# Optimization experiments

Hardware: AMD Instinct MI355X
Metric: run time of the kernel (lower is better)

Reference implementation:

```python
import jax, jax.numpy as jnp
import numpy as np

N_NODES = 50000
N_EDGES = 600000
D_IN = 128
D_OUT = 128


def setup_inputs() -> dict:
    key = jax.random.key(0)
    ks = jax.random.split(key, 6)
    gain = float(np.sqrt(2.0))  # relu gain for xavier init
    lim = gain * np.sqrt(6.0 / (D_IN + D_IN))
    pool_w = jax.random.uniform(ks[0], (D_IN, D_IN), jnp.float32, -lim, lim)
    lim2 = gain * np.sqrt(6.0 / (D_IN + D_OUT))
    lin_w = jax.random.uniform(ks[1], (D_OUT, D_IN), jnp.float32, -lim2, lim2)
    return {
        "node_feats": jax.random.normal(ks[2], (N_NODES, D_IN), jnp.float32),
        "src": jax.random.randint(ks[3], (N_EDGES,), 0, N_NODES, jnp.int32),
        "dst": jax.random.randint(ks[4], (N_EDGES,), 0, N_NODES, jnp.int32),
        "e_weight": jax.random.uniform(ks[5], (N_EDGES,), jnp.float32),
        "pool_w": pool_w,
        "pool_b": jnp.zeros((D_IN,), jnp.float32),
        "lin_w": lin_w,
        "lin_b": jnp.zeros((D_OUT,), jnp.float32),
        "bias": jnp.zeros((D_OUT,), jnp.float32),
    }


def reference(node_feats, src, dst, e_weight, pool_w, pool_b, lin_w, lin_b, bias):
    # maxpool aggregator: h_src = relu(pool(x) + pool_bias)   [N, D_IN]
    h_src = jax.nn.relu(node_feats @ pool_w.T + pool_b)
    # u_mul_e message: gather src features, scale by edge weight  [E, D_IN]
    m = h_src[src] * e_weight[:, None]
    # fn.max reduce per destination node; empty mailboxes -> 0
    h_new = jax.ops.segment_max(m, dst, num_segments=N_NODES)
    h_new = jnp.where(jnp.isfinite(h_new), h_new, 0.0)
    # final linear (+its bias) + extra bias parameter
    return h_new @ lin_w.T + lin_b + bias
```

## Files before the change

### kernel.cpp

```cpp
#include <hip/hip_runtime.h>
#include <hip/hip_bf16.h>

#define NN 50000
#define NE 600000
#define DD 128
#define CAP 48

typedef __attribute__((ext_vector_type(8))) short short8_t;
typedef __attribute__((ext_vector_type(4))) short short4_t;
typedef __attribute__((ext_vector_type(4))) float f32x4;

__device__ __forceinline__ short f2bf(float f) {
    union { float f; unsigned u; } v; v.f = f;
    unsigned r = (v.u + 0x7FFFu + ((v.u >> 16) & 1u)) >> 16;
    return (short)r;
}
__device__ __forceinline__ float bflo(unsigned x) { return __uint_as_float(x << 16); }
__device__ __forceinline__ float bfhi(unsigned x) { return __uint_as_float(x & 0xffff0000u); }

template<bool RELU, bool B2, bool IN_BF, bool OUT_BF>
__global__ __launch_bounds__(512) void gemm128(const void* __restrict__ Av,
        const float* __restrict__ W, const float* __restrict__ b1,
        const float* __restrict__ b2, void* __restrict__ outv, int M,
        int* __restrict__ zbuf)
{
    __shared__ short aL[128 * 128];
    __shared__ short wL[128 * 128];
    const int tid = threadIdx.x;
    const int m0 = blockIdx.x * 128;

    if (zbuf) {
        int gid = blockIdx.x * 512 + tid;
        if (gid < NN) zbuf[gid] = 0;
    }

    if (IN_BF) {
        const unsigned short* A = (const unsigned short*)Av;
        #pragma unroll
        for (int i = 0; i < 4; ++i) {
            int flat = i * 4096 + tid * 8;
            int row = flat >> 7, k = flat & 127;
            int gr = m0 + row;
            short8_t s8 = {0,0,0,0,0,0,0,0};
            if (gr < M) s8 = *(const short8_t*)(A + (size_t)gr * 128 + k);
            *(short8_t*)(aL + ((row * 128 + k) ^ ((row & 7) << 3))) = s8;
        }
    } else {
        const float* A = (const float*)Av;
        #pragma unroll
        for (int i = 0; i < 8; ++i) {
            int flat = i * 2048 + tid * 4;
            int row = flat >> 7, k = flat & 127;
            int gr = m0 + row;
            float4 v = make_float4(0.f, 0.f, 0.f, 0.f);
            if (gr < M) v = *(const float4*)(A + (size_t)gr * 128 + k);
            short4_t s4 = { f2bf(v.x), f2bf(v.y), f2bf(v.z), f2bf(v.w) };
            *(short4_t*)(aL + ((row * 128 + k) ^ ((row & 7) << 3))) = s4;
        }
    }
    #pragma unroll
    for (int i = 0; i < 8; ++i) {
        int flat = i * 2048 + tid * 4;
        int row = flat >> 7, k = flat & 127;
        float4 v = *(const float4*)(W + flat);
        short4_t s4 = { f2bf(v.x), f2bf(v.y), f2bf(v.z), f2bf(v.w) };
        *(short4_t*)(wL + ((row * 128 + k) ^ ((row & 7) << 3))) = s4;
    }
    __syncthreads();

    const int lane = tid & 63, wid = tid >> 6;
    const int l15 = lane & 15, lhi = lane >> 4;
    const int r0 = wid * 16;
    f32x4 acc[8];
    #pragma unroll
    for (int t = 0; t < 8; ++t) acc[t] = f32x4{0.f, 0.f, 0.f, 0.f};

    #pragma unroll
    for (int kk = 0; kk < 4; ++kk) {
        const int k0 = kk * 32 + lhi * 8;
        const int ar = r0 + l15;
        short8_t a = *(short8_t*)(aL + ((ar * 128 + k0) ^ ((ar & 7) << 3)));
        #pragma unroll
        for (int t = 0; t < 8; ++t) {
            const int br = t * 16 + l15;
            short8_t b = *(short8_t*)(wL + ((br * 128 + k0) ^ ((br & 7) << 3)));
            acc[t] = __builtin_amdgcn_mfma_f32_16x16x32_bf16(a, b, acc[t], 0, 0, 0);
        }
    }

    #pragma unroll
    for (int t = 0; t < 8; ++t) {
        const int c = t * 16 + l15;
        float add = b1[c];
        if (B2) add += b2[c];
        #pragma unroll
        for (int i = 0; i < 4; ++i) {
            int r = m0 + r0 + lhi * 4 + i;
            if (r < M) {
                float v = acc[t][i] + add;
                if (RELU) v = fmaxf(v, 0.f);
                if (OUT_BF) ((unsigned short*)outv)[(size_t)r * 128 + c] = (unsigned short)f2bf(v);
                else        ((float*)outv)[(size_t)r * 128 + c] = v;
            }
        }
    }
}

__global__ __launch_bounds__(256) void bucket(const int* __restrict__ src,
        const int* __restrict__ dst, const float* __restrict__ ew,
        int* __restrict__ counts, unsigned* __restrict__ edges)
{
    int e = blockIdx.x * 256 + threadIdx.x;
    if (e >= NE) return;
    int d = dst[e];
    int pos = atomicAdd(&counts[d], 1);
    if (pos < CAP)
        edges[(size_t)d * CAP + pos] =
            ((unsigned)src[e] << 16) | (unsigned short)f2bf(ew[e]);
}

__global__ __launch_bounds__(256) void node_max(const unsigned short* __restrict__ hb,
        const int* __restrict__ counts, const unsigned* __restrict__ edges,
        unsigned short* __restrict__ hnew)
{
    int node = blockIdx.x * 4 + (threadIdx.x >> 6);
    if (node >= NN) return;
    const int lane = threadIdx.x & 63;
    const int g = lane >> 4, l16 = lane & 15;
    const int deg = min(counts[node], CAP);
    const unsigned* ep = edges + (size_t)node * CAP;
    unsigned p = (lane < deg) ? ep[lane] : 0u;

    float m0=0.f,m1=0.f,m2=0.f,m3=0.f,m4=0.f,m5=0.f,m6=0.f,m7=0.f;
    for (int j = 0; j < deg; j += 8) {
        int ia = j + g, ib = j + 4 + g;
        unsigned pa = __shfl(p, ia & 63);
        unsigned pb = __shfl(p, ib & 63);
        float wa = (ia < deg) ? __uint_as_float(pa << 16) : 0.f;
        float wb = (ib < deg) ? __uint_as_float(pb << 16) : 0.f;
        uint4 ra = *(const uint4*)(hb + (size_t)(pa >> 16) * 128 + l16 * 8);
        uint4 rb = *(const uint4*)(hb + (size_t)(pb >> 16) * 128 + l16 * 8);
        m0 = fmaxf(m0, bflo(ra.x) * wa); m1 = fmaxf(m1, bfhi(ra.x) * wa);
        m2 = fmaxf(m2, bflo(ra.y) * wa); m3 = fmaxf(m3, bfhi(ra.y) * wa);
        m4 = fmaxf(m4, bflo(ra.z) * wa); m5 = fmaxf(m5, bfhi(ra.z) * wa);
        m6 = fmaxf(m6, bflo(ra.w) * wa); m7 = fmaxf(m7, bfhi(ra.w) * wa);
        m0 = fmaxf(m0, bflo(rb.x) * wb); m1 = fmaxf(m1, bfhi(rb.x) * wb);
        m2 = fmaxf(m2, bflo(rb.y) * wb); m3 = fmaxf(m3, bfhi(rb.y) * wb);
        m4 = fmaxf(m4, bflo(rb.z) * wb); m5 = fmaxf(m5, bfhi(rb.z) * wb);
        m6 = fmaxf(m6, bflo(rb.w) * wb); m7 = fmaxf(m7, bfhi(rb.w) * wb);
    }

    #define CMB(mm) mm = fmaxf(mm, __shfl_xor(mm, 16)); \
                    mm = fmaxf(mm, __shfl_xor(mm, 32));
    CMB(m0) CMB(m1) CMB(m2) CMB(m3) CMB(m4) CMB(m5) CMB(m6) CMB(m7)
    #undef CMB

    if (g == 0) {
        uint4 o;
        o.x = ((unsigned)(unsigned short)f2bf(m1) << 16) | (unsigned short)f2bf(m0);
        o.y = ((unsigned)(unsigned short)f2bf(m3) << 16) | (unsigned short)f2bf(m2);
        o.z = ((unsigned)(unsigned short)f2bf(m5) << 16) | (unsigned short)f2bf(m4);
        o.w = ((unsigned)(unsigned short)f2bf(m7) << 16) | (unsigned short)f2bf(m6);
        *(uint4*)(hnew + (size_t)node * 128 + l16 * 8) = o;
    }
}

extern "C" void kernel_launch(void* const* d_in, const int* in_sizes, int n_in,
                              void* d_out, int out_size, void* d_ws, size_t ws_size,
                              hipStream_t stream) {
    const float* node_feats = (const float*)d_in[0];
    const int*   src        = (const int*)d_in[1];
    const int*   dst        = (const int*)d_in[2];
    const float* ew         = (const float*)d_in[3];
    const float* pool_w     = (const float*)d_in[4];
    const float* pool_b     = (const float*)d_in[5];
    const float* lin_w      = (const float*)d_in[6];
    const float* lin_b      = (const float*)d_in[7];
    const float* bias       = (const float*)d_in[8];
    float* out = (float*)d_out;

    char* w0 = (char*)d_ws;
    unsigned short* hsrc = (unsigned short*)w0;  w0 += (size_t)NN * DD * 2;
    unsigned short* hnew = (unsigned short*)w0;  w0 += (size_t)NN * DD * 2;
    int* counts = (int*)w0;                      w0 += (size_t)NN * 4;
    unsigned* edges = (unsigned*)w0;             w0 += (size_t)NN * CAP * 4;

    const int gemm_grid = (NN + 127) / 128;
    gemm128<true, false, false, true><<<gemm_grid, 512, 0, stream>>>(node_feats,
            pool_w, pool_b, nullptr, hsrc, NN, counts);

    bucket<<<(NE + 255) / 256, 256, 0, stream>>>(src, dst, ew, counts, edges);

    node_max<<<(NN + 3) / 4, 256, 0, stream>>>(hsrc, counts, edges, hnew);

    gemm128<false, true, true, false><<<gemm_grid, 512, 0, stream>>>(hnew,
            lin_w, lin_b, bias, out, NN, nullptr);
}
```

Measured before the change: 167.8 us.

## Pre-convert weights to bf16, load GEMM operands into registers, unroll gather by degree

A new prep kernel converts both weight matrices to bf16 once and zeroes the per-node edge counters. The GEMM is rewritten to read A and B fragments straight from global memory into registers, dropping the LDS staging and barrier, and uses 64-row tiles with waves split across column halves. The node_max gather now runs a fully unrolled loop whose iteration count (2, 4 or 6) is picked by degree bucket, so more loads can be in flight. The costs are an extra kernel launch and redundant weight-fragment loads per wave that rely on the cache to absorb them.

Measured after the change: 195.9 us. 16.8% more time.

```diff
diff --git a/kernel.cpp b/kernel.cpp
--- a/kernel.cpp
+++ b/kernel.cpp
@@ -18,84 +18,86 @@
 __device__ __forceinline__ float bflo(unsigned x) { return __uint_as_float(x << 16); }
 __device__ __forceinline__ float bfhi(unsigned x) { return __uint_as_float(x & 0xffff0000u); }
 
+__global__ __launch_bounds__(256) void prep(const float* __restrict__ pw,
+        const float* __restrict__ lw, unsigned short* __restrict__ w1,
+        unsigned short* __restrict__ w2, int* __restrict__ counts)
+{
+    const int b = blockIdx.x, t = threadIdx.x;
+    if (b < 196) {
+        int i = b * 256 + t;
+        if (i < NN) counts[i] = 0;
+    } else if (b < 212) {
+        int base = (b - 196) * 1024 + t * 4;
+        float4 v = *(const float4*)(pw + base);
+        short4_t s4 = { f2bf(v.x), f2bf(v.y), f2bf(v.z), f2bf(v.w) };
+        *(short4_t*)(w1 + base) = s4;
+    } else {
+        int base = (b - 212) * 1024 + t * 4;
+        float4 v = *(const float4*)(lw + base);
+        short4_t s4 = { f2bf(v.x), f2bf(v.y), f2bf(v.z), f2bf(v.w) };
+        *(short4_t*)(w2 + base) = s4;
+    }
+}
+
 template<bool RELU, bool B2, bool IN_BF, bool OUT_BF>
-__global__ __launch_bounds__(512) void gemm128(const void* __restrict__ Av,
-        const float* __restrict__ W, const float* __restrict__ b1,
-        const float* __restrict__ b2, void* __restrict__ outv, int M,
-        int* __restrict__ zbuf)
-{
-    __shared__ short aL[128 * 128];
-    __shared__ short wL[128 * 128];
+__global__ __launch_bounds__(512) void gemmz(const void* __restrict__ Av,
+        const unsigned short* __restrict__ Wb, const float* __restrict__ b1,
+        const float* __restrict__ b2, void* __restrict__ outv, int M)
+{
     const int tid = threadIdx.x;
-    const int m0 = blockIdx.x * 128;
-
-    if (zbuf) {
-        int gid = blockIdx.x * 512 + tid;
-        if (gid < NN) zbuf[gid] = 0;
-    }
-
+    const int lane = tid & 63, wid = tid >> 6;
+    const int l15 = lane & 15, lhi = lane >> 4;
+    const int rg = wid & 3, cs = wid >> 2;
+    const int m0 = blockIdx.x * 64 + rg * 16;
+    const int ar = m0 + l15;
+
+    short8_t bf[4][4];
+    #pragma unroll
+    for (int t = 0; t < 4; ++t) {
+        const int br = cs * 64 + t * 16 + l15;
+        #pragma unroll
+        for (int kk = 0; kk < 4; ++kk)
+            bf[t][kk] = *(const short8_t*)(Wb + br * 128 + kk * 32 + lhi * 8);
+    }
+
+    short8_t af[4];
     if (IN_BF) {
         const unsigned short* A = (const unsigned short*)Av;
         #pragma unroll
-        for (int i = 0; i < 4; ++i) {
-            int flat = i * 4096 + tid * 8;
-            int row = flat >> 7, k = flat & 127;
-            int gr = m0 + row;
-            short8_t s8 = {0,0,0,0,0,0,0,0};
-            if (gr < M) s8 = *(const short8_t*)(A + (size_t)gr * 128 + k);
-            *(short8_t*)(aL + ((row * 128 + k) ^ ((row & 7) << 3))) = s8;
+        for (int kk = 0; kk < 4; ++kk)
+            af[kk] = *(const short8_t*)(A + (size_t)ar * 128 + kk * 32 + lhi * 8);
+    } else {
+        const int arc = min(ar, M - 1);
+        const float* A = (const float*)Av;
+        #pragma unroll
+        for (int kk = 0; kk < 4; ++kk) {
+            float4 u = *(const float4*)(A + (size_t)arc * 128 + kk * 32 + lhi * 8);
+            float4 v = *(const float4*)(A + (size_t)arc * 128 + kk * 32 + lhi * 8 + 4);
+            af[kk] = short8_t{ f2bf(u.x), f2bf(u.y), f2bf(u.z), f2bf(u.w),
+                               f2bf(v.x), f2bf(v.y), f2bf(v.z), f2bf(v.w) };
         }
-    } else {
-        const float* A = (const float*)Av;
-        #pragma unroll
-        for (int i = 0; i < 8; ++i) {
-            int flat = i * 2048 + tid * 4;
-            int row = flat >> 7, k = flat & 127;
-            int gr = m0 + row;
-            float4 v = make_float4(0.f, 0.f, 0.f, 0.f);
-            if (gr < M) v = *(const float4*)(A + (size_t)gr * 128 + k);
-            short4_t s4 = { f2bf(v.x), f2bf(v.y), f2bf(v.z), f2bf(v.w) };
-            *(short4_t*)(aL + ((row * 128 + k) ^ ((row & 7) << 3))) = s4;
-        }
-    }
-    #pragma unroll
-    for (int i = 0; i < 8; ++i) {
-        int flat = i * 2048 + tid * 4;
-        int row = flat >> 7, k = flat & 127;
-        float4 v = *(const float4*)(W + flat);
-        short4_t s4 = { f2bf(v.x), f2bf(v.y), f2bf(v.z), f2bf(v.w) };
-        *(short4_t*)(wL + ((row * 128 + k) ^ ((row & 7) << 3))) = s4;
-    }
-    __syncthreads();
-
-    const int lane = tid & 63, wid = tid >> 6;
-    const int l15 = lane & 15, lhi = lane >> 4;
-    const int r0 = wid * 16;
-    f32x4 acc[8];
-    #pragma unroll
-    for (int t = 0; t < 8; ++t) acc[t] = f32x4{0.f, 0.f, 0.f, 0.f};
+    }
+
+    f32x4 acc[4];
+    #pragma unroll
+    for (int t = 0; t < 4; ++t) acc[t] = f32x4{0.f, 0.f, 0.f, 0.f};
 
     #pragma unroll
     for (int kk = 0; kk < 4; ++kk) {
-        const int k0 = kk * 32 + lhi * 8;
-        const int ar = r0 + l15;
-        short8_t a = *(short8_t*)(aL + ((ar * 128 + k0) ^ ((ar & 7) << 3)));
-        #pragma unroll
-        for (int t = 0; t < 8; ++t) {
-            const int br = t * 16 + l15;
-            short8_t b = *(short8_t*)(wL + ((br * 128 + k0) ^ ((br & 7) << 3)));
-            acc[t] = __builtin_amdgcn_mfma_f32_16x16x32_bf16(a, b, acc[t], 0, 0, 0);
-        }
-    }
-
-    #pragma unroll
-    for (int t = 0; t < 8; ++t) {
-        const int c = t * 16 + l15;
+        #pragma unroll
+        for (int t = 0; t < 4; ++t)
+            acc[t] = __builtin_amdgcn_mfma_f32_16x16x32_bf16(af[kk], bf[t][kk],
+                                                             acc[t], 0, 0, 0);
+    }
+
+    #pragma unroll
+    for (int t = 0; t < 4; ++t) {
+        const int c = cs * 64 + t * 16 + l15;
         float add = b1[c];
         if (B2) add += b2[c];
         #pragma unroll
         for (int i = 0; i < 4; ++i) {
-            int r = m0 + r0 + lhi * 4 + i;
+            int r = m0 + lhi * 4 + i;
             if (r < M) {
                 float v = acc[t][i] + add;
                 if (RELU) v = fmaxf(v, 0.f);
@@ -119,6 +121,29 @@
             ((unsigned)src[e] << 16) | (unsigned short)f2bf(ew[e]);
 }
 
+template<int NIT>
+__device__ __forceinline__ void gat(const unsigned short* __restrict__ hb,
+        unsigned p, int deg, int g, int l16, float* m)
+{
+    #pragma unroll
+    for (int it = 0; it < NIT; ++it) {
+        const int ia = it * 8 + g, ib = it * 8 + 4 + g;
+        unsigned pa = __shfl(p, ia), pb = __shfl(p, ib);
+        float wa = (ia < deg) ? __uint_as_float(pa << 16) : 0.f;
+        float wb = (ib < deg) ? __uint_as_float(pb << 16) : 0.f;
+        uint4 ra = *(const uint4*)(hb + (size_t)(pa >> 16) * 128 + l16 * 8);
+        uint4 rb = *(const uint4*)(hb + (size_t)(pb >> 16) * 128 + l16 * 8);
+        m[0] = fmaxf(m[0], bflo(ra.x) * wa); m[1] = fmaxf(m[1], bfhi(ra.x) * wa);
+        m[2] = fmaxf(m[2], bflo(ra.y) * wa); m[3] = fmaxf(m[3], bfhi(ra.y) * wa);
+        m[4] = fmaxf(m[4], bflo(ra.z) * wa); m[5] = fmaxf(m[5], bfhi(ra.z) * wa);
+        m[6] = fmaxf(m[6], bflo(ra.w) * wa); m[7] = fmaxf(m[7], bfhi(ra.w) * wa);
+        m[0] = fmaxf(m[0], bflo(rb.x) * wb); m[1] = fmaxf(m[1], bfhi(rb.x) * wb);
+        m[2] = fmaxf(m[2], bflo(rb.y) * wb); m[3] = fmaxf(m[3], bfhi(rb.y) * wb);
+        m[4] = fmaxf(m[4], bflo(rb.z) * wb); m[5] = fmaxf(m[5], bfhi(rb.z) * wb);
+        m[6] = fmaxf(m[6], bflo(rb.w) * wb); m[7] = fmaxf(m[7], bfhi(rb.w) * wb);
+    }
+}
+
 __global__ __launch_bounds__(256) void node_max(const unsigned short* __restrict__ hb,
         const int* __restrict__ counts, const unsigned* __restrict__ edges,
         unsigned short* __restrict__ hnew)
@@ -131,36 +156,26 @@
     const unsigned* ep = edges + (size_t)node * CAP;
     unsigned p = (lane < deg) ? ep[lane] : 0u;
 
-    float m0=0.f,m1=0.f,m2=0.f,m3=0.f,m4=0.f,m5=0.f,m6=0.f,m7=0.f;
-    for (int j = 0; j < deg; j += 8) {
-        int ia = j + g, ib = j + 4 + g;
-        unsigned pa = __shfl(p, ia & 63);
-        unsigned pb = __shfl(p, ib & 63);
-        float wa = (ia < deg) ? __uint_as_float(pa << 16) : 0.f;
-        float wb = (ib < deg) ? __uint_as_float(pb << 16) : 0.f;
-        uint4 ra = *(const uint4*)(hb + (size_t)(pa >> 16) * 128 + l16 * 8);
-        uint4 rb = *(const uint4*)(hb + (size_t)(pb >> 16) * 128 + l16 * 8);
-        m0 = fmaxf(m0, bflo(ra.x) * wa); m1 = fmaxf(m1, bfhi(ra.x) * wa);
-        m2 = fmaxf(m2, bflo(ra.y) * wa); m3 = fmaxf(m3, bfhi(ra.y) * wa);
-        m4 = fmaxf(m4, bflo(ra.z) * wa); m5 = fmaxf(m5, bfhi(ra.z) * wa);
-        m6 = fmaxf(m6, bflo(ra.w) * wa); m7 = fmaxf(m7, bfhi(ra.w) * wa);
-        m0 = fmaxf(m0, bflo(rb.x) * wb); m1 = fmaxf(m1, bfhi(rb.x) * wb);
-        m2 = fmaxf(m2, bflo(rb.y) * wb); m3 = fmaxf(m3, bfhi(rb.y) * wb);
-        m4 = fmaxf(m4, bflo(rb.z) * wb); m5 = fmaxf(m5, bfhi(rb.z) * wb);
-        m6 = fmaxf(m6, bflo(rb.w) * wb); m7 = fmaxf(m7, bfhi(rb.w) * wb);
-    }
-
-    #define CMB(mm) mm = fmaxf(mm, __shfl_xor(mm, 16)); \
-                    mm = fmaxf(mm, __shfl_xor(mm, 32));
-    CMB(m0) CMB(m1) CMB(m2) CMB(m3) CMB(m4) CMB(m5) CMB(m6) CMB(m7)
-    #undef CMB
+    float m[8];
+    #pragma unroll
+    for (int i = 0; i < 8; ++i) m[i] = 0.f;
+
+    if (deg <= 16)      gat<2>(hb, p, deg, g, l16, m);
+    else if (deg <= 32) gat<4>(hb, p, deg, g, l16, m);
+    else                gat<6>(hb, p, deg, g, l16, m);
+
+    #pragma unroll
+    for (int i = 0; i < 8; ++i) {
+        m[i] = fmaxf(m[i], __shfl_xor(m[i], 16));
+        m[i] = fmaxf(m[i], __shfl_xor(m[i], 32));
+    }
 
     if (g == 0) {
         uint4 o;
-        o.x = ((unsigned)(unsigned short)f2bf(m1) << 16) | (unsigned short)f2bf(m0);
-        o.y = ((unsigned)(unsigned short)f2bf(m3) << 16) | (unsigned short)f2bf(m2);
-        o.z = ((unsigned)(unsigned short)f2bf(m5) << 16) | (unsigned short)f2bf(m4);
-        o.w = ((unsigned)(unsigned short)f2bf(m7) << 16) | (unsigned short)f2bf(m6);
+        o.x = ((unsigned)(unsigned short)f2bf(m[1]) << 16) | (unsigned short)f2bf(m[0]);
+        o.y = ((unsigned)(unsigned short)f2bf(m[3]) << 16) | (unsigned short)f2bf(m[2]);
+        o.z = ((unsigned)(unsigned short)f2bf(m[5]) << 16) | (unsigned short)f2bf(m[4]);
+        o.w = ((unsigned)(unsigned short)f2bf(m[7]) << 16) | (unsigned short)f2bf(m[6]);
         *(uint4*)(hnew + (size_t)node * 128 + l16 * 8) = o;
     }
 }
@@ -184,15 +199,19 @@
     unsigned short* hnew = (unsigned short*)w0;  w0 += (size_t)NN * DD * 2;
     int* counts = (int*)w0;                      w0 += (size_t)NN * 4;
     unsigned* edges = (unsigned*)w0;             w0 += (size_t)NN * CAP * 4;
-
-    const int gemm_grid = (NN + 127) / 128;
-    gemm128<true, false, false, true><<<gemm_grid, 512, 0, stream>>>(node_feats,
-            pool_w, pool_b, nullptr, hsrc, NN, counts);
+    unsigned short* w1b = (unsigned short*)w0;   w0 += (size_t)DD * DD * 2;
+    unsigned short* w2b = (unsigned short*)w0;   w0 += (size_t)DD * DD * 2;
+
+    prep<<<228, 256, 0, stream>>>(pool_w, lin_w, w1b, w2b, counts);
+
+    const int gz_grid = (NN + 63) / 64;
+    gemmz<true, false, false, true><<<gz_grid, 512, 0, stream>>>(node_feats,
+            w1b, pool_b, nullptr, hsrc, NN);
 
     bucket<<<(NE + 255) / 256, 256, 0, stream>>>(src, dst, ew, counts, edges);
 
     node_max<<<(NN + 3) / 4, 256, 0, stream>>>(hsrc, counts, edges, hnew);
 
-    gemm128<false, true, true, false><<<gemm_grid, 512, 0, stream>>>(hnew,
-            lin_w, lin_b, bias, out, NN, nullptr);
-}
+    gemmz<false, true, true, false><<<gz_grid, 512, 0, stream>>>(hnew,
+            w2b, lin_b, bias, out, NN);
+}
```
